# Performance work log

Measured on AMD Instinct MI355X. Metric: run time of the kernel, lower is better.

## Reference

```python
import jax, jax.numpy as jnp
import numpy as np

B, D, H, W = 32, 256, 32, 32
K = 1024

def setup_inputs() -> dict:
    key = jax.random.key(0)
    k1, k2 = jax.random.split(key)
    x = jax.random.normal(k1, (B, D, H, W), dtype=jnp.float32)
    codebook = jax.random.normal(k2, (K, D), dtype=jnp.float32)
    return {"x": x, "codebook": codebook}

def reference(x, codebook):
    b, lat, h, w = x.shape
    # (B, D, H, W) -> (B*H*W, D) tokens
    xt = jnp.transpose(x, (0, 2, 3, 1)).reshape(-1, lat)  # [N, D]
    # Squared euclidean distances via expansion (argmin-equivalent to cdist)
    x_sq = jnp.sum(xt * xt, axis=-1, keepdims=True)           # [N, 1]
    c_sq = jnp.sum(codebook * codebook, axis=-1)[None, :]     # [1, K]
    dist2 = x_sq - 2.0 * (xt @ codebook.T) + c_sq             # [N, K]
    idx = jnp.argmin(dist2, axis=-1)                          # [N]
    quant = codebook[idx]                                     # [N, D]
    codebook_loss = jnp.mean((jax.lax.stop_gradient(xt) - quant) ** 2)
    commitment_loss = jnp.mean((xt - jax.lax.stop_gradient(quant)) ** 2)
    # Straight-through estimator
    out = xt + jax.lax.stop_gradient(quant - xt)              # [N, D]
    out = out.reshape(b, h, w, lat).transpose(0, 3, 1, 2)     # [B, D, H, W]
    min_enc_idx = idx.reshape(b, h, w)                        # [B, H, W]
    return out, min_enc_idx, codebook_loss, commitment_loss
```

## Files before the change

### kernel.cpp

```cpp
#include <hip/hip_runtime.h>

#define B_   32
#define D_   256
#define HW_  1024
#define N_   32768
#define K_   1024
#define DHW  (D_ * HW_)
#define MARGIN 0.3f

typedef __attribute__((ext_vector_type(8)))  short bf16x8;
typedef __attribute__((ext_vector_type(16))) float f32x16;

union FragU { uint4 q; bf16x8 v; };

__device__ inline uint bf16rne(float x) {
    uint ub = __float_as_uint(x);
    return (ub + 0x7fffu + ((ub >> 16) & 1u)) >> 16;
}

__global__ __launch_bounds__(256)
void prep_cb(const float* __restrict__ cb, uint4* __restrict__ cbt2,
             float* __restrict__ csq, int* __restrict__ rcount,
             float* __restrict__ oloss) {
    __shared__ uint sh[256], sl[256];
    __shared__ float rr[4];
    const int k = blockIdx.x, d = threadIdx.x;
    float v = cb[(size_t)k * D_ + d];
    uint hb = bf16rne(v);
    float hf = __uint_as_float(hb << 16);
    uint lb = bf16rne(v - hf);
    sh[d] = hb; sl[d] = lb;
    float s = v * v;
    #pragma unroll
    for (int off = 32; off >= 1; off >>= 1) s += __shfl_xor(s, off, 64);
    if ((d & 63) == 0) rr[d >> 6] = s;
    __syncthreads();
    if (d == 0) csq[k] = (rr[0] + rr[1]) + (rr[2] + rr[3]);
    if (k == 0 && d == 0) { *rcount = 0; oloss[0] = 0.f; oloss[1] = 0.f; }
    if (d < 64) {
        const int ch = d >> 2, it = d & 3;
        const int p = it >> 1, h = it & 1;
        const int d0 = ch * 16 + h * 8;
        const uint* src = p ? sl : sh;
        uint w[4];
        #pragma unroll
        for (int jj = 0; jj < 4; ++jj)
            w[jj] = src[d0 + 2 * jj] | (src[d0 + 2 * jj + 1] << 16);
        cbt2[((ch * 4 + it) << 10) + k] = make_uint4(w[0], w[1], w[2], w[3]);
    }
}

#define DO_STEP(SA, SB, SC, SD, S) do {                                          \
    const int cc_ = cq * 4 + (S);                                                \
    const int ch_ = cc_ & 15;                                                    \
    FragU tf[4];                                                                 \
    _Pragma("unroll")                                                            \
    for (int j = 0; j < 4; ++j) tf[j].q = TkS[ch_ * 2 + sub][j * 32 + l31];      \
    __builtin_amdgcn_s_setprio(1);                                               \
    _Pragma("unroll")                                                            \
    for (int j = 0; j < 4; ++j)                                                  \
        acc[0][j] = __builtin_amdgcn_mfma_f32_32x32x16_bf16(SA.v, tf[j].v, acc[0][j], 0, 0, 0); \
    _Pragma("unroll")                                                            \
    for (int j = 0; j < 4; ++j)                                                  \
        acc[1][j] = __builtin_amdgcn_mfma_f32_32x32x16_bf16(SB.v, tf[j].v, acc[1][j], 0, 0, 0); \
    _Pragma("unroll")                                                            \
    for (int j = 0; j < 4; ++j)                                                  \
        acc[0][j] = __builtin_amdgcn_mfma_f32_32x32x16_bf16(SC.v, tf[j].v, acc[0][j], 0, 0, 0); \
    _Pragma("unroll")                                                            \
    for (int j = 0; j < 4; ++j)                                                  \
        acc[1][j] = __builtin_amdgcn_mfma_f32_32x32x16_bf16(SD.v, tf[j].v, acc[1][j], 0, 0, 0); \
    __builtin_amdgcn_s_setprio(0);                                               \
    if (cq < 7) {                                                                \
        const int nc_ = cc_ + 4;                                                 \
        const int noff_ = (((nc_ & 15) * 4) << 10) + ((nc_ >> 4) * 64);          \
        SA.q = cb_hi[noff_];      SB.q = cb_hi[noff_ + 32];                      \
        SC.q = cb_lo[noff_];      SD.q = cb_lo[noff_ + 32];                      \
    }                                                                            \
} while (0)

__global__ __launch_bounds__(512, 1)
void vq_main(const float* __restrict__ x, const uint4* __restrict__ cbt2,
             const float* __restrict__ csqg, const float* __restrict__ cb,
             int* __restrict__ rcount, int* __restrict__ rlist,
             float* __restrict__ bdist, float* __restrict__ out,
             float* __restrict__ oidx, float* __restrict__ oloss) {
    __shared__ uint4 TkS[32][128];
    __shared__ float csqS[1024];

    const int tid = threadIdx.x;
    const int lane = tid & 63;
    const int sub = lane >> 5, l31 = lane & 31;
    const int w = tid >> 6;
    const int tok0 = blockIdx.x * 128;
    const int bb = tok0 >> 10, hw0 = tok0 & 1023;

    csqS[tid] = csqg[tid];
    csqS[tid + 512] = csqg[tid + 512];

    const uint4* cb_hi = cbt2 + (sub << 10) + w * 128 + l31;
    const uint4* cb_lo = cbt2 + ((2 + sub) << 10) + w * 128 + l31;

    FragU p0a, p0b, p0c, p0d, p1a, p1b, p1c, p1d,
          p2a, p2b, p2c, p2d, p3a, p3b, p3c, p3d;
    p0a.q = cb_hi[0];         p0b.q = cb_hi[32];
    p0c.q = cb_lo[0];         p0d.q = cb_lo[32];
    p1a.q = cb_hi[1 << 12];   p1b.q = cb_hi[(1 << 12) + 32];
    p1c.q = cb_lo[1 << 12];   p1d.q = cb_lo[(1 << 12) + 32];
    p2a.q = cb_hi[2 << 12];   p2b.q = cb_hi[(2 << 12) + 32];
    p2c.q = cb_lo[2 << 12];   p2d.q = cb_lo[(2 << 12) + 32];
    p3a.q = cb_hi[3 << 12];   p3b.q = cb_hi[(3 << 12) + 32];
    p3c.q = cb_lo[3 << 12];   p3d.q = cb_lo[(3 << 12) + 32];

    {
        const int t = tid & 127;
        const int dgrp = tid >> 7;
        const float* xp = x + (size_t)bb * DHW + hw0 + t;
        #pragma unroll
        for (int i = 0; i < 8; ++i) {
            int g = i * 4 + dgrp;
            float v[8];
            #pragma unroll
            for (int e = 0; e < 8; ++e)
                v[e] = xp[(size_t)(g * 8 + e) * HW_];
            uint wd[4];
            #pragma unroll
            for (int jj = 0; jj < 4; ++jj)
                wd[jj] = bf16rne(v[2 * jj]) | (bf16rne(v[2 * jj + 1]) << 16);
            TkS[g][t] = make_uint4(wd[0], wd[1], wd[2], wd[3]);
        }
    }
    __syncthreads();

    f32x16 acc[2][4] = {};
    float v1[4], v2[4]; int k1[4];
    #pragma unroll
    for (int j = 0; j < 4; ++j) { v1[j] = 3.4e38f; v2[j] = 3.4e38f; k1[j] = 0; }

    for (int cq = 0; cq < 8; ++cq) {
        DO_STEP(p0a, p0b, p0c, p0d, 0);
        DO_STEP(p1a, p1b, p1c, p1d, 1);
        DO_STEP(p2a, p2b, p2c, p2d, 2);
        DO_STEP(p3a, p3b, p3c, p3d, 3);

        if ((cq & 3) == 3) {
            const int ct = cq >> 2;
            const int cbase = w * 128 + ct * 64 + sub * 4;
            #pragma unroll
            for (int f = 0; f < 2; ++f) {
                #pragma unroll
                for (int g8 = 0; g8 < 4; ++g8) {
                    float4 cs4 = *reinterpret_cast<const float4*>(&csqS[cbase + f * 32 + g8 * 8]);
                    const float csa[4] = {cs4.x, cs4.y, cs4.z, cs4.w};
                    #pragma unroll
                    for (int q = 0; q < 4; ++q) {
                        int code = cbase + f * 32 + g8 * 8 + q;
                        int r = g8 * 4 + q;
                        #pragma unroll
                        for (int j = 0; j < 4; ++j) {
                            float s = fmaf(-2.f, acc[f][j][r], csa[q]);
                            bool c = s < v1[j];
                            v2[j] = c ? v1[j] : fminf(v2[j], s);
                            k1[j] = c ? code : k1[j];
                            v1[j] = c ? s : v1[j];
                        }
                    }
                }
            }
            const f32x16 zf = {};
            #pragma unroll
            for (int f = 0; f < 2; ++f)
                #pragma unroll
                for (int j = 0; j < 4; ++j) acc[f][j] = zf;
        }
    }

    #pragma unroll
    for (int j = 0; j < 4; ++j) {
        float ov1 = __shfl_xor(v1[j], 32, 64);
        float ov2 = __shfl_xor(v2[j], 32, 64);
        int   ok1 = __shfl_xor(k1[j], 32, 64);
        float nv2 = fminf(fminf(v2[j], ov2), fmaxf(v1[j], ov1));
        if (ov1 < v1[j] || (ov1 == v1[j] && ok1 < k1[j])) { v1[j] = ov1; k1[j] = ok1; }
        v2[j] = nv2;
    }
    __syncthreads();
    float* red = (float*)&TkS[0][0];
    int* bestk_s = (int*)(red + 3072);
    if (sub == 0) {
        #pragma unroll
        for (int j = 0; j < 4; ++j) {
            int t = j * 32 + l31;
            red[(w * 128 + t) * 3 + 0] = v1[j];
            red[(w * 128 + t) * 3 + 1] = v2[j];
            red[(w * 128 + t) * 3 + 2] = __int_as_float(k1[j]);
        }
    }
    __syncthreads();
    if (tid < 128) {
        float bv1 = red[tid * 3], bv2 = red[tid * 3 + 1];
        int bk = __float_as_int(red[tid * 3 + 2]);
        #pragma unroll
        for (int m = 1; m < 8; ++m) {
            float a1 = red[(m * 128 + tid) * 3], a2 = red[(m * 128 + tid) * 3 + 1];
            int ak = __float_as_int(red[(m * 128 + tid) * 3 + 2]);
            float nv2 = fminf(fminf(bv2, a2), fmaxf(bv1, a1));
            if (a1 < bv1 || (a1 == bv1 && ak < bk)) { bv1 = a1; bk = ak; }
            bv2 = nv2;
        }
        int n = tok0 + tid;
        bestk_s[tid] = bk;
        bdist[n] = bv1;
        oidx[n] = (float)bk;
        if (bv2 - bv1 < MARGIN) rlist[atomicAdd(rcount, 1)] = n;
        float v = bv1;
        #pragma unroll
        for (int off = 32; off >= 1; off >>= 1) v += __shfl_xor(v, off, 64);
        if ((tid & 63) == 0) {
            float t2 = v * (1.0f / 8388608.0f);
            atomicAdd(&oloss[0], t2);
            atomicAdd(&oloss[1], t2);
        }
    }
    __syncthreads();

    {
        const int j32 = tid & 31, dg = tid >> 5;
        int k4[4];
        #pragma unroll
        for (int e = 0; e < 4; ++e) k4[e] = bestk_s[j32 * 4 + e];
        const size_t obase = (size_t)bb * DHW + hw0 + j32 * 4;
        #pragma unroll 4
        for (int d = dg * 16; d < dg * 16 + 16; ++d) {
            float4 wv;
            wv.x = cb[(size_t)k4[0] * D_ + d];
            wv.y = cb[(size_t)k4[1] * D_ + d];
            wv.z = cb[(size_t)k4[2] * D_ + d];
            wv.w = cb[(size_t)k4[3] * D_ + d];
            *reinterpret_cast<float4*>(out + obase + (size_t)d * HW_) = wv;
        }
    }
}

__global__ __launch_bounds__(1024)
void vq_refine(const float* __restrict__ x, const float* __restrict__ cb,
               const float* __restrict__ csq, const int* __restrict__ rcount,
               const int* __restrict__ rlist, const float* __restrict__ bdist,
               float* __restrict__ out, float* __restrict__ oidx,
               float* __restrict__ oloss) {
    __shared__ float xv[8][256];
    __shared__ float xsq[8];
    __shared__ float wredv[16][8];
    __shared__ int   wredk[16][8];
    __shared__ int   kfin[8];
    const int tid = threadIdx.x;
    const int code = tid;
    const int wv_i = tid >> 6, lane = tid & 63;
    const int cnt = min(rcount[0], N_);
    for (int base = blockIdx.x * 8; base < cnt; base += gridDim.x * 8) {
        const int m = min(8, cnt - base);
        __syncthreads();
        {
            const int j = tid >> 8, d = tid & 255;
            #pragma unroll
            for (int rep = 0; rep < 2; ++rep) {
                int jj = j + rep * 4;
                float val = 0.f;
                if (jj < m) {
                    int n = rlist[base + jj];
                    int b = n >> 10, hw = n & 1023;
                    val = x[(size_t)b * DHW + (size_t)d * HW_ + hw];
                }
                xv[jj][d] = val;
            }
        }
        __syncthreads();
        if (tid < 256) {
            int g = tid >> 5, l = tid & 31;
            float s = 0.f;
            #pragma unroll
            for (int d8 = 0; d8 < 8; ++d8) { float v = xv[g][d8 * 32 + l]; s = fmaf(v, v, s); }
            #pragma unroll
            for (int mm = 1; mm < 32; mm <<= 1) s += __shfl_xor(s, mm, 64);
            if (l == 0) xsq[g] = s;
        }
        __syncthreads();

        float dot[8];
        #pragma unroll
        for (int j = 0; j < 8; ++j) dot[j] = 0.f;

        const float* crow = cb + (size_t)code * D_;
        for (int d0 = 0; d0 < 256; d0 += 8) {
            float xr[8][8];
            #pragma unroll
            for (int j = 0; j < 8; ++j) {
                float4 a = *reinterpret_cast<const float4*>(&xv[j][d0]);
                float4 b = *reinterpret_cast<const float4*>(&xv[j][d0 + 4]);
                xr[j][0] = a.x; xr[j][1] = a.y; xr[j][2] = a.z; xr[j][3] = a.w;
                xr[j][4] = b.x; xr[j][5] = b.y; xr[j][6] = b.z; xr[j][7] = b.w;
            }
            const float4* cr = reinterpret_cast<const float4*>(crow + d0);
            float4 ca = cr[0], cbv = cr[1];
            float cv[8] = { ca.x, ca.y, ca.z, ca.w, cbv.x, cbv.y, cbv.z, cbv.w };
            #pragma unroll
            for (int u = 0; u < 8; ++u)
                #pragma unroll
                for (int j = 0; j < 8; ++j)
                    dot[j] = fmaf(cv[u], xr[j][u], dot[j]);
        }

        const float cs = csq[code];
        #pragma unroll
        for (int j = 0; j < 8; ++j) {
            if (j < m) {
                float v = fmaf(-2.f, dot[j], xsq[j]) + cs;
                int k = code;
                #pragma unroll
                for (int mm = 1; mm < 64; mm <<= 1) {
                    float ov = __shfl_xor(v, mm, 64);
                    int   ok = __shfl_xor(k, mm, 64);
                    if (ov < v || (ov == v && ok < k)) { v = ov; k = ok; }
                }
                if (lane == 0) { wredv[wv_i][j] = v; wredk[wv_i][j] = k; }
            }
        }
        __syncthreads();
        if (tid < m) {
            float v = wredv[0][tid]; int k = wredk[0][tid];
            #pragma unroll
            for (int q = 1; q < 16; ++q) {
                if (wredv[q][tid] < v || (wredv[q][tid] == v && wredk[q][tid] < k)) {
                    v = wredv[q][tid]; k = wredk[q][tid];
                }
            }
            int n = rlist[base + tid];
            kfin[tid] = k;
            oidx[n] = (float)k;
            float delta = (v - bdist[n]) * (1.0f / 8388608.0f);
            atomicAdd(&oloss[0], delta);
            atomicAdd(&oloss[1], delta);
        }
        __syncthreads();
        {
            const int j = tid >> 8, d = tid & 255;
            #pragma unroll
            for (int rep = 0; rep < 2; ++rep) {
                int jj = j + rep * 4;
                if (jj < m) {
                    int n = rlist[base + jj];
                    int b = n >> 10, hw = n & 1023;
                    out[(size_t)b * DHW + (size_t)d * HW_ + hw] = cb[(size_t)kfin[jj] * D_ + d];
                }
            }
        }
        __syncthreads();
    }
}

extern "C" void kernel_launch(void* const* d_in, const int* in_sizes, int n_in,
                              void* d_out, int out_size, void* d_ws, size_t ws_size,
                              hipStream_t stream) {
    const float* x  = (const float*)d_in[0];
    const float* cb = (const float*)d_in[1];

    float* out   = (float*)d_out;
    float* oidx  = out + 8388608;
    float* oloss = out + 8388608 + 32768;

    uint* wsb = (uint*)d_ws;
    uint4*  cbt2  = (uint4*)wsb;
    float*  csq   = (float*)(wsb + 262144);
    int*    rcount= (int*)  (wsb + 263168);
    int*    rlist = (int*)  (wsb + 263172);
    float*  bdist = (float*)(wsb + 295940);

    prep_cb <<<1024, 256, 0, stream>>>(cb, cbt2, csq, rcount, oloss);
    vq_main <<<256, 512, 0, stream>>>(x, cbt2, csq, cb, rcount, rlist, bdist, out, oidx, oloss);
    vq_refine<<<128, 1024, 0, stream>>>(x, cb, csq, rcount, rlist, bdist, out, oidx, oloss);
}
```

Baseline: 119.4 us.

## Stage gathered codebook rows in LDS and read transposed codebook in refine

The output scatter in vq_main first gathers the chosen codebook rows into shared memory with contiguous float4 loads, then writes transposed float4 stores to the NCHW output. This replaces the strided per-element global gathers of the old version. prep_cb also writes a transposed codebook (D x K), so vq_refine reads it coalesced across threads instead of each thread reading its own row. In exchange it adds a 1 MB workspace write, an extra scattered store in prep_cb, and two more block barriers.

```diff
diff --git a/kernel.cpp b/kernel.cpp
--- a/kernel.cpp
+++ b/kernel.cpp
@@ -20,8 +20,8 @@
 
 __global__ __launch_bounds__(256)
 void prep_cb(const float* __restrict__ cb, uint4* __restrict__ cbt2,
-             float* __restrict__ csq, int* __restrict__ rcount,
-             float* __restrict__ oloss) {
+             float* __restrict__ csq, float* __restrict__ cbT,
+             int* __restrict__ rcount, float* __restrict__ oloss) {
     __shared__ uint sh[256], sl[256];
     __shared__ float rr[4];
     const int k = blockIdx.x, d = threadIdx.x;
@@ -30,6 +30,7 @@
     float hf = __uint_as_float(hb << 16);
     uint lb = bf16rne(v - hf);
     sh[d] = hb; sl[d] = lb;
+    cbT[(size_t)d * K_ + k] = v;
     float s = v * v;
     #pragma unroll
     for (int off = 32; off >= 1; off >>= 1) s += __shfl_xor(s, off, 64);
@@ -84,8 +85,9 @@
              int* __restrict__ rcount, int* __restrict__ rlist,
              float* __restrict__ bdist, float* __restrict__ out,
              float* __restrict__ oidx, float* __restrict__ oloss) {
-    __shared__ uint4 TkS[32][128];
-    __shared__ float csqS[1024];
+    __shared__ __align__(16) uint SMEM[17408];
+    uint4 (*TkS)[128] = reinterpret_cast<uint4(*)[128]>(SMEM);
+    float* csqS = reinterpret_cast<float*>(SMEM + 16384);
 
     const int tid = threadIdx.x;
     const int lane = tid & 63;
@@ -184,8 +186,8 @@
         v2[j] = nv2;
     }
     __syncthreads();
-    float* red = (float*)&TkS[0][0];
-    int* bestk_s = (int*)(red + 3072);
+    float* red = reinterpret_cast<float*>(SMEM);
+    int* bestk_s = reinterpret_cast<int*>(SMEM + 17280);
     if (sub == 0) {
         #pragma unroll
         for (int j = 0; j < 4; ++j) {
@@ -223,30 +225,41 @@
     }
     __syncthreads();
 
-    {
-        const int j32 = tid & 31, dg = tid >> 5;
-        int k4[4];
-        #pragma unroll
-        for (int e = 0; e < 4; ++e) k4[e] = bestk_s[j32 * 4 + e];
-        const size_t obase = (size_t)bb * DHW + hw0 + j32 * 4;
-        #pragma unroll 4
-        for (int d = dg * 16; d < dg * 16 + 16; ++d) {
-            float4 wv;
-            wv.x = cb[(size_t)k4[0] * D_ + d];
-            wv.y = cb[(size_t)k4[1] * D_ + d];
-            wv.z = cb[(size_t)k4[2] * D_ + d];
-            wv.w = cb[(size_t)k4[3] * D_ + d];
-            *reinterpret_cast<float4*>(out + obase + (size_t)d * HW_) = wv;
-        }
+    float* S2 = reinterpret_cast<float*>(SMEM);
+    #pragma unroll 1
+    for (int h = 0; h < 2; ++h) {
+        #pragma unroll
+        for (int i = 0; i < 8; ++i) {
+            int r = w * 8 + i;
+            int kk = bestk_s[h * 64 + r];
+            float4 cw4 = *reinterpret_cast<const float4*>(cb + (size_t)kk * D_ + lane * 4);
+            *reinterpret_cast<float4*>(&S2[r * 260 + lane * 4]) = cw4;
+        }
+        __syncthreads();
+        {
+            const int q = tid & 15, dg = tid >> 4;
+            const size_t obase = (size_t)bb * DHW + hw0 + h * 64 + q * 4;
+            #pragma unroll
+            for (int dd = 0; dd < 8; ++dd) {
+                int d = dg * 8 + dd;
+                float4 wv;
+                wv.x = S2[(q * 4 + 0) * 260 + d];
+                wv.y = S2[(q * 4 + 1) * 260 + d];
+                wv.z = S2[(q * 4 + 2) * 260 + d];
+                wv.w = S2[(q * 4 + 3) * 260 + d];
+                *reinterpret_cast<float4*>(out + obase + (size_t)d * HW_) = wv;
+            }
+        }
+        __syncthreads();
     }
 }
 
 __global__ __launch_bounds__(1024)
 void vq_refine(const float* __restrict__ x, const float* __restrict__ cb,
-               const float* __restrict__ csq, const int* __restrict__ rcount,
-               const int* __restrict__ rlist, const float* __restrict__ bdist,
-               float* __restrict__ out, float* __restrict__ oidx,
-               float* __restrict__ oloss) {
+               const float* __restrict__ cbT, const float* __restrict__ csq,
+               const int* __restrict__ rcount, const int* __restrict__ rlist,
+               const float* __restrict__ bdist, float* __restrict__ out,
+               float* __restrict__ oidx, float* __restrict__ oloss) {
     __shared__ float xv[8][256];
     __shared__ float xsq[8];
     __shared__ float wredv[16][8];
@@ -289,7 +302,6 @@
         #pragma unroll
         for (int j = 0; j < 8; ++j) dot[j] = 0.f;
 
-        const float* crow = cb + (size_t)code * D_;
         for (int d0 = 0; d0 < 256; d0 += 8) {
             float xr[8][8];
             #pragma unroll
@@ -299,9 +311,10 @@
                 xr[j][0] = a.x; xr[j][1] = a.y; xr[j][2] = a.z; xr[j][3] = a.w;
                 xr[j][4] = b.x; xr[j][5] = b.y; xr[j][6] = b.z; xr[j][7] = b.w;
             }
-            const float4* cr = reinterpret_cast<const float4*>(crow + d0);
-            float4 ca = cr[0], cbv = cr[1];
-            float cv[8] = { ca.x, ca.y, ca.z, ca.w, cbv.x, cbv.y, cbv.z, cbv.w };
+            float cv[8];
+            #pragma unroll
+            for (int u = 0; u < 8; ++u)
+                cv[u] = cbT[(size_t)(d0 + u) * K_ + code];
             #pragma unroll
             for (int u = 0; u < 8; ++u)
                 #pragma unroll
@@ -370,11 +383,12 @@
     uint* wsb = (uint*)d_ws;
     uint4*  cbt2  = (uint4*)wsb;
     float*  csq   = (float*)(wsb + 262144);
-    int*    rcount= (int*)  (wsb + 263168);
-    int*    rlist = (int*)  (wsb + 263172);
-    float*  bdist = (float*)(wsb + 295940);
-
-    prep_cb <<<1024, 256, 0, stream>>>(cb, cbt2, csq, rcount, oloss);
+    float*  cbT   = (float*)(wsb + 263168);
+    int*    rcount= (int*)  (wsb + 525312);
+    int*    rlist = (int*)  (wsb + 525316);
+    float*  bdist = (float*)(wsb + 558084);
+
+    prep_cb <<<1024, 256, 0, stream>>>(cb, cbt2, csq, cbT, rcount, oloss);
     vq_main <<<256, 512, 0, stream>>>(x, cbt2, csq, cb, rcount, rlist, bdist, out, oidx, oloss);
-    vq_refine<<<128, 1024, 0, stream>>>(x, cb, csq, rcount, rlist, bdist, out, oidx, oloss);
-}
+    vq_refine<<<128, 1024, 0, stream>>>(x, cb, cbT, csq, rcount, rlist, bdist, out, oidx, oloss);
+}
```

New measurement: 107.3 us. 10.1% less time.
